# Kernel optimization log

Measured on AMD Instinct MI355X. Metric: run time of the kernel, lower is better.

## Reference

```python
import jax, jax.numpy as jnp
import numpy as np

NUM_HEADS = 16

def setup_inputs() -> dict:
    key = jax.random.key(0)
    ks = jax.random.split(key, 7)
    query_dim, kv_dim, out_dim = 1024, 768, 1024
    N, Lq, Lkv = 4, 2048, 2048
    s_q = 1.0 / np.sqrt(query_dim)
    s_kv = 1.0 / np.sqrt(kv_dim)
    return {
        "query": jax.random.normal(ks[0], (N, Lq, query_dim), dtype=jnp.float32),
        "kv": jax.random.normal(ks[1], (N, Lkv, kv_dim), dtype=jnp.float32),
        # Linear weights stored as (in_dim, out_dim) for x @ W
        "Wq": jax.random.uniform(ks[2], (query_dim, query_dim), jnp.float32, -s_q, s_q),
        "Wk": jax.random.uniform(ks[3], (kv_dim, query_dim), jnp.float32, -s_kv, s_kv),
        "Wv": jax.random.uniform(ks[4], (kv_dim, query_dim), jnp.float32, -s_kv, s_kv),
        "Wo": jax.random.uniform(ks[5], (query_dim, out_dim), jnp.float32, -s_q, s_q),
        "bo": jax.random.uniform(ks[6], (out_dim,), jnp.float32, -s_q, s_q),
    }

def reference(query, kv, Wq, Wk, Wv, Wo, bo):
    N, Lq, qd = query.shape
    Lkv = kv.shape[1]
    H = NUM_HEADS
    hd = qd // H
    scale = hd ** -0.5
    # projections -> (N, H, L, hd)
    q = (query @ Wq).reshape(N, Lq, H, hd).transpose(0, 2, 1, 3)
    k = (kv @ Wk).reshape(N, Lkv, H, hd).transpose(0, 2, 1, 3)
    v = (kv @ Wv).reshape(N, Lkv, H, hd).transpose(0, 2, 1, 3)
    # fp32 attention: (N, H, Lq, Lkv)
    attn = jnp.einsum('bhqd,bhkd->bhqk', q.astype(jnp.float32) * scale, k.astype(jnp.float32))
    attn = jax.nn.softmax(attn, axis=-1)
    out = jnp.einsum('bhqk,bhkd->bhqd', attn, v.astype(jnp.float32))
    out = out.transpose(0, 2, 1, 3).reshape(N, Lq, qd)
    return out @ Wo + bo
```

## Files before the change

### kernel.cpp

```cpp
#include <hip/hip_runtime.h>

typedef __attribute__((ext_vector_type(4))) float f32x4;
typedef __attribute__((ext_vector_type(8))) __bf16 bf16x8;
typedef __attribute__((ext_vector_type(8))) unsigned short us8;

__device__ __forceinline__ unsigned short f2bf(float f) {
    unsigned u = __builtin_bit_cast(unsigned, f);
    u += 0x7fffu + ((u >> 16) & 1u);
    return (unsigned short)(u >> 16);
}

__device__ __forceinline__ float exp2v(float x) {
    float r;
    asm("v_exp_f32 %0, %1" : "=v"(r) : "v"(x));
    return r;
}

__device__ __forceinline__ f32x4 mfma16(bf16x8 a, bf16x8 b, f32x4 c) {
    return __builtin_amdgcn_mfma_f32_16x16x32_bf16(a, b, c, 0, 0, 0);
}

__device__ __forceinline__ void gload16(const void* g, void* l) {
    __builtin_amdgcn_global_load_lds(
        (const __attribute__((address_space(1))) unsigned int*)g,
        (__attribute__((address_space(3))) unsigned int*)l, 16, 0, 0);
}

__global__ __launch_bounds__(256) void conv2_bf16(const float* __restrict__ a,
                                                  unsigned short* __restrict__ oa,
                                                  int na8,
                                                  const float* __restrict__ b,
                                                  unsigned short* __restrict__ ob,
                                                  int nb8) {
    int i = blockIdx.x * 256 + threadIdx.x;
    const float* in;
    unsigned short* out;
    if (i < na8) {
        in = a; out = oa;
    } else {
        i -= na8;
        if (i >= nb8) return;
        in = b; out = ob;
    }
    const float4* p = (const float4*)in + (size_t)i * 2;
    float4 x = p[0], y = p[1];
    us8 o;
    o[0] = f2bf(x.x); o[1] = f2bf(x.y); o[2] = f2bf(x.z); o[3] = f2bf(x.w);
    o[4] = f2bf(y.x); o[5] = f2bf(y.y); o[6] = f2bf(y.z); o[7] = f2bf(y.w);
    *((us8*)out + i) = o;
}

__global__ __launch_bounds__(256) void wtrans_all(const float* __restrict__ Wq,
                                                  const float* __restrict__ Wk,
                                                  const float* __restrict__ Wv,
                                                  const float* __restrict__ Wo,
                                                  unsigned short* __restrict__ WqT,
                                                  unsigned short* __restrict__ WkT,
                                                  unsigned short* __restrict__ WvT,
                                                  unsigned short* __restrict__ WoT,
                                                  float qscale) {
    __shared__ float t[32][33];
    int y = blockIdx.y;
    const float* in; unsigned short* out; int R; float scale = 1.0f;
    if (y < 32)      { in = Wq; out = WqT; R = 1024; scale = qscale; }
    else if (y < 56) { in = Wk; out = WkT; R = 768;  y -= 32; }
    else if (y < 80) { in = Wv; out = WvT; R = 768;  y -= 56; }
    else             { in = Wo; out = WoT; R = 1024; y -= 80; }
    int tx = threadIdx.x, ty = threadIdx.y;
    int r0 = y * 32, c0 = blockIdx.x * 32;
#pragma unroll
    for (int k = 0; k < 4; ++k)
        t[ty + k * 8][tx] = in[(size_t)(r0 + ty + k * 8) * 1024 + c0 + tx];
    __syncthreads();
#pragma unroll
    for (int k = 0; k < 4; ++k)
        out[(size_t)(c0 + ty + k * 8) * R + r0 + tx] = f2bf(t[tx][ty + k * 8] * scale);
}

template <int KD, int EPI>
__global__ __launch_bounds__(256, 4) void gemm_bf16(const unsigned short* __restrict__ A,
                                                    const unsigned short* __restrict__ B,
                                                    void* __restrict__ Cout,
                                                    const float* __restrict__ bias) {
    __shared__ __align__(16) unsigned short SL[2][8192];
    const int m0 = blockIdx.y * 128;
    const int n0 = blockIdx.x * 128;
    const int tid = threadIdx.x;
    const int w = tid >> 6, l = tid & 63;
    const int lr = l & 15, lg = l >> 4;
    const int wm = (w >> 1) * 64, wn = (w & 1) * 64;

    f32x4 acc[4][4] = {};

    int ci0 = w * 64 + l;
    int r0 = ci0 >> 2, c0 = (ci0 & 3) ^ (r0 & 3);
    int ci1 = 256 + ci0;
    int r1 = ci1 >> 2, c1 = (ci1 & 3) ^ (r1 & 3);

    const unsigned short* Ag0 = A + (size_t)(m0 + r0) * KD + c0 * 8;
    const unsigned short* Ag1 = A + (size_t)(m0 + r1) * KD + c1 * 8;
    const unsigned short* Bg0 = B + (size_t)(n0 + r0) * KD + c0 * 8;
    const unsigned short* Bg1 = B + (size_t)(n0 + r1) * KD + c1 * 8;

#define STG(buf, k0)                                                  \
    do {                                                              \
        gload16(Ag0 + (k0), &SL[buf][w * 512]);                       \
        gload16(Ag1 + (k0), &SL[buf][2048 + w * 512]);                \
        gload16(Bg0 + (k0), &SL[buf][4096 + w * 512]);                \
        gload16(Bg1 + (k0), &SL[buf][4096 + 2048 + w * 512]);         \
    } while (0)

    constexpr int NT = KD / 32;
    STG(0, 0);
    int buf = 0;
    for (int kt = 0; kt < NT; ++kt) {
        if (kt + 1 < NT) {
            STG(buf ^ 1, (kt + 1) * 32);
            asm volatile("s_waitcnt vmcnt(4)" ::: "memory");
        } else {
            asm volatile("s_waitcnt vmcnt(0)" ::: "memory");
        }
        __builtin_amdgcn_s_barrier();
        const unsigned short* Alc = &SL[buf][0];
        const unsigned short* Blc = &SL[buf][4096];
        bf16x8 af[4], bfr[4];
#pragma unroll
        for (int t = 0; t < 4; ++t) {
            int ar = wm + t * 16 + lr;
            af[t] = *(const bf16x8*)&Alc[ar * 32 + ((lg ^ (ar & 3)) * 8)];
            int br = wn + t * 16 + lr;
            bfr[t] = *(const bf16x8*)&Blc[br * 32 + ((lg ^ (br & 3)) * 8)];
        }
#pragma unroll
        for (int i = 0; i < 4; ++i)
#pragma unroll
            for (int j = 0; j < 4; ++j)
                acc[i][j] = mfma16(af[i], bfr[j], acc[i][j]);
        __builtin_amdgcn_s_barrier();
        buf ^= 1;
    }
#undef STG

#pragma unroll
    for (int i = 0; i < 4; ++i)
#pragma unroll
        for (int j = 0; j < 4; ++j)
#pragma unroll
            for (int r = 0; r < 4; ++r) {
                int m = m0 + wm + i * 16 + lg * 4 + r;
                int n = n0 + wn + j * 16 + lr;
                if (EPI == 0) {
                    int b = m >> 11, ql = m & 2047, h = n >> 6, d = n & 63;
                    ((unsigned short*)Cout)[(((size_t)(b * 16 + h) * 2048 + ql) << 6) + d] =
                        f2bf(acc[i][j][r]);
                } else {
                    ((float*)Cout)[(size_t)m * 1024 + n] = acc[i][j][r] + bias[n];
                }
            }
}

__global__ __launch_bounds__(256, 4) void gemm_kv(const unsigned short* __restrict__ A,
                                                  const unsigned short* __restrict__ Bk,
                                                  const unsigned short* __restrict__ Bv,
                                                  unsigned short* __restrict__ Ck,
                                                  unsigned short* __restrict__ Cv) {
    constexpr int KD = 768;
    __shared__ __align__(16) unsigned short SL[2][8192];
    const int isV = blockIdx.x >> 3;
    const int n0 = (blockIdx.x & 7) * 128;
    const int m0 = blockIdx.y * 128;
    const unsigned short* B = isV ? Bv : Bk;
    const int tid = threadIdx.x;
    const int w = tid >> 6, l = tid & 63;
    const int lr = l & 15, lg = l >> 4;
    const int wm = (w >> 1) * 64, wn = (w & 1) * 64;

    f32x4 acc[4][4] = {};

    int ci0 = w * 64 + l;
    int r0 = ci0 >> 2, c0 = (ci0 & 3) ^ (r0 & 3);
    int ci1 = 256 + ci0;
    int r1 = ci1 >> 2, c1 = (ci1 & 3) ^ (r1 & 3);

    const unsigned short* Ag0 = A + (size_t)(m0 + r0) * KD + c0 * 8;
    const unsigned short* Ag1 = A + (size_t)(m0 + r1) * KD + c1 * 8;
    const unsigned short* Bg0 = B + (size_t)(n0 + r0) * KD + c0 * 8;
    const unsigned short* Bg1 = B + (size_t)(n0 + r1) * KD + c1 * 8;

#define STG(buf, k0)                                                  \
    do {                                                              \
        gload16(Ag0 + (k0), &SL[buf][w * 512]);                       \
        gload16(Ag1 + (k0), &SL[buf][2048 + w * 512]);                \
        gload16(Bg0 + (k0), &SL[buf][4096 + w * 512]);                \
        gload16(Bg1 + (k0), &SL[buf][4096 + 2048 + w * 512]);         \
    } while (0)

    constexpr int NT = KD / 32;
    STG(0, 0);
    int buf = 0;
    for (int kt = 0; kt < NT; ++kt) {
        if (kt + 1 < NT) {
            STG(buf ^ 1, (kt + 1) * 32);
            asm volatile("s_waitcnt vmcnt(4)" ::: "memory");
        } else {
            asm volatile("s_waitcnt vmcnt(0)" ::: "memory");
        }
        __builtin_amdgcn_s_barrier();
        const unsigned short* Alc = &SL[buf][0];
        const unsigned short* Blc = &SL[buf][4096];
        bf16x8 af[4], bfr[4];
#pragma unroll
        for (int t = 0; t < 4; ++t) {
            int ar = wm + t * 16 + lr;
            af[t] = *(const bf16x8*)&Alc[ar * 32 + ((lg ^ (ar & 3)) * 8)];
            int br = wn + t * 16 + lr;
            bfr[t] = *(const bf16x8*)&Blc[br * 32 + ((lg ^ (br & 3)) * 8)];
        }
#pragma unroll
        for (int i = 0; i < 4; ++i)
#pragma unroll
            for (int j = 0; j < 4; ++j)
                acc[i][j] = mfma16(af[i], bfr[j], acc[i][j]);
        __builtin_amdgcn_s_barrier();
        buf ^= 1;
    }
#undef STG

    if (!isV) {
#pragma unroll
        for (int i = 0; i < 4; ++i)
#pragma unroll
            for (int j = 0; j < 4; ++j)
#pragma unroll
                for (int r = 0; r < 4; ++r) {
                    int m = m0 + wm + i * 16 + lg * 4 + r;
                    int n = n0 + wn + j * 16 + lr;
                    int b = m >> 11, ql = m & 2047, h = n >> 6, d = n & 63;
                    Ck[(((size_t)(b * 16 + h) * 2048 + ql) << 6) + d] = f2bf(acc[i][j][r]);
                }
    } else {
        const int b = m0 >> 11;
        const int mloc = m0 & 2047;
        const int h0 = n0 >> 6;
#pragma unroll
        for (int hp = 0; hp < 2; ++hp) {
            unsigned short* VTb = Cv + (size_t)(b * 16 + h0 + hp) * (64 * 2048);
#pragma unroll
            for (int dh = 0; dh < 2; ++dh) {
                __syncthreads();
                if ((w & 1) == hp) {
#pragma unroll
                    for (int jj = 0; jj < 2; ++jj) {
                        int j = dh * 2 + jj;
                        int dl = jj * 16 + lr;
#pragma unroll
                        for (int i = 0; i < 4; ++i)
#pragma unroll
                            for (int r = 0; r < 4; ++r) {
                                int kvl = wm + i * 16 + lg * 4 + r;
                                int pl = (kvl & 0x60) | (((kvl >> 2) & 3) << 3) |
                                         (((kvl >> 4) & 1) << 2) | (kvl & 3);
                                SL[0][dl * 136 + pl] = f2bf(acc[i][j][r]);
                            }
                    }
                }
                __syncthreads();
#pragma unroll
                for (int cc = 0; cc < 2; ++cc) {
                    int idx = cc * 256 + tid;
                    int row = idx >> 4, col = (idx & 15) * 8;
                    *(us8*)&VTb[(size_t)(dh * 32 + row) * 2048 + mloc + col] =
                        *(const us8*)&SL[0][row * 136 + col];
                }
            }
        }
    }
}

__global__ __launch_bounds__(256, 4) void attn_fwd(const unsigned short* __restrict__ Q,
                                                   const unsigned short* __restrict__ K,
                                                   const unsigned short* __restrict__ VT,
                                                   unsigned short* __restrict__ O) {
    __shared__ __align__(16) unsigned short Kl[2][64 * 64];
    __shared__ __align__(16) unsigned short Vl[2][64 * 64];
    const int id = blockIdx.x;
    const int sw = (id & 7) * 128 + (id >> 3);
    const int qt = sw & 15, bh = sw >> 4;
    const int tid = threadIdx.x;
    const int w = tid >> 6, l = tid & 63;
    const int lr = l & 15, lg = l >> 4;
    const size_t hbase = (size_t)bh * (2048 * 64);
    const size_t vbase = (size_t)bh * (64 * 2048);
    const int qbase = qt * 128 + w * 32;

    bf16x8 qf[2][2];
#pragma unroll
    for (int rt = 0; rt < 2; ++rt) {
        const unsigned short* qp = Q + hbase + (size_t)(qbase + rt * 16 + lr) * 64;
        qf[rt][0] = *(const bf16x8*)(qp + lg * 8);
        qf[rt][1] = *(const bf16x8*)(qp + 32 + lg * 8);
    }

    f32x4 oacc[2][4] = {};
    f32x4 lacc[2] = {};
    const f32x4 FZERO = {};

    bf16x8 ONES;
#pragma unroll
    for (int e = 0; e < 8; ++e) ONES[e] = (__bf16)1.0f;

    const int cA = tid, cB = 256 + tid;
    const int krA = cA >> 3, kcA = (cA & 7) ^ (krA & 7);
    const int krB = cB >> 3, kcB = (cB & 7) ^ (krB & 7);
    const unsigned short* Kg0 = K + hbase + (size_t)krA * 64 + kcA * 8;
    const unsigned short* Kg1 = K + hbase + (size_t)krB * 64 + kcB * 8;
    const unsigned short* Vg0 = VT + vbase + (size_t)krA * 2048 + kcA * 8;
    const unsigned short* Vg1 = VT + vbase + (size_t)krB * 2048 + kcB * 8;

#define STAGE_KV(dst, kv0)                                                    \
    do {                                                                      \
        gload16(Kg0 + (size_t)(kv0) * 64, &Kl[dst][w * 512]);                 \
        gload16(Kg1 + (size_t)(kv0) * 64, &Kl[dst][2048 + w * 512]);          \
        gload16(Vg0 + (kv0), &Vl[dst][w * 512]);                              \
        gload16(Vg1 + (kv0), &Vl[dst][2048 + w * 512]);                       \
    } while (0)

    const int koff0 = lr * 64 + ((lg ^ (lr & 7)) * 8);
    const int koff1 = lr * 64 + (((4 + lg) ^ (lr & 7)) * 8);

    STAGE_KV(0, 0);
    int cur = 0;

    for (int t = 0; t < 32; ++t) {
        if (t < 31) {
            STAGE_KV(cur ^ 1, (t + 1) * 64);
            asm volatile("s_waitcnt vmcnt(4)" ::: "memory");
        } else {
            asm volatile("s_waitcnt vmcnt(0)" ::: "memory");
        }
        __builtin_amdgcn_s_barrier();
        const unsigned short* Kc = Kl[cur];
        const unsigned short* Vc = Vl[cur];

        f32x4 s[2][4];
        __builtin_amdgcn_s_setprio(1);
#pragma unroll
        for (int nt = 0; nt < 4; ++nt) {
            bf16x8 kf0 = *(const bf16x8*)&Kc[koff0 + nt * 1024];
            bf16x8 kf1 = *(const bf16x8*)&Kc[koff1 + nt * 1024];
            s[0][nt] = mfma16(kf0, qf[0][0], FZERO);
            s[0][nt] = mfma16(kf1, qf[0][1], s[0][nt]);
            s[1][nt] = mfma16(kf0, qf[1][0], FZERO);
            s[1][nt] = mfma16(kf1, qf[1][1], s[1][nt]);
        }
        __builtin_amdgcn_s_setprio(0);

        bf16x8 pa0[2], pa1[2];
#pragma unroll
        for (int rt = 0; rt < 2; ++rt) {
#pragma unroll
            for (int nt = 0; nt < 4; ++nt)
#pragma unroll
                for (int r = 0; r < 4; ++r)
                    s[rt][nt][r] = exp2v(s[rt][nt][r]);
#pragma unroll
            for (int e = 0; e < 4; ++e) {
                pa0[rt][e] = (__bf16)s[rt][0][e];
                pa0[rt][4 + e] = (__bf16)s[rt][1][e];
                pa1[rt][e] = (__bf16)s[rt][2][e];
                pa1[rt][4 + e] = (__bf16)s[rt][3][e];
            }
        }

        __builtin_amdgcn_s_setprio(1);
        lacc[0] = mfma16(pa0[0], ONES, lacc[0]);
        lacc[0] = mfma16(pa1[0], ONES, lacc[0]);
        lacc[1] = mfma16(pa0[1], ONES, lacc[1]);
        lacc[1] = mfma16(pa1[1], ONES, lacc[1]);

#pragma unroll
        for (int nt = 0; nt < 4; ++nt) {
            bf16x8 vb0 = *(const bf16x8*)&Vc[koff0 + nt * 1024];
            bf16x8 vb1 = *(const bf16x8*)&Vc[koff1 + nt * 1024];
            oacc[0][nt] = mfma16(pa0[0], vb0, oacc[0][nt]);
            oacc[0][nt] = mfma16(pa1[0], vb1, oacc[0][nt]);
            oacc[1][nt] = mfma16(pa0[1], vb0, oacc[1][nt]);
            oacc[1][nt] = mfma16(pa1[1], vb1, oacc[1][nt]);
        }
        __builtin_amdgcn_s_setprio(0);
        __builtin_amdgcn_s_barrier();
        cur ^= 1;
    }
#undef STAGE_KV

    const int b = bh >> 4, h = bh & 15;
#pragma unroll
    for (int rt = 0; rt < 2; ++rt)
#pragma unroll
        for (int r = 0; r < 4; ++r) {
            float inv = 1.0f / lacc[rt][r];
            int q = qbase + rt * 16 + lg * 4 + r;
            size_t rowbase = ((size_t)(b * 2048 + q)) * 1024 + h * 64;
#pragma unroll
            for (int nt = 0; nt < 4; ++nt)
                O[rowbase + nt * 16 + lr] = f2bf(oacc[rt][nt][r] * inv);
        }
}

extern "C" void kernel_launch(void* const* d_in, const int* in_sizes, int n_in,
                              void* d_out, int out_size, void* d_ws, size_t ws_size,
                              hipStream_t stream) {
    (void)in_sizes; (void)n_in; (void)out_size; (void)ws_size;
    const float* query = (const float*)d_in[0];
    const float* kv    = (const float*)d_in[1];
    const float* Wq    = (const float*)d_in[2];
    const float* Wk    = (const float*)d_in[3];
    const float* Wv    = (const float*)d_in[4];
    const float* Wo    = (const float*)d_in[5];
    const float* bo    = (const float*)d_in[6];
    float* out = (float*)d_out;

    char* ws = (char*)d_ws;
    unsigned short* qbf  = (unsigned short*)(ws + 0);
    unsigned short* kvbf = (unsigned short*)(ws + 16777216);
    unsigned short* WkT  = (unsigned short*)(ws + 29360128);
    unsigned short* WvT  = (unsigned short*)(ws + 30932992);
    unsigned short* WqT  = (unsigned short*)(ws + 32505856);
    unsigned short* WoT  = (unsigned short*)(ws + 34603008);
    unsigned short* Qh   = (unsigned short*)(ws + 36700160);
    unsigned short* Kh   = (unsigned short*)(ws + 53477376);
    unsigned short* VTh  = (unsigned short*)(ws + 0);
    unsigned short* Ob   = (unsigned short*)(ws + 16777216);

    const float QSCALE = 0.18033688011112042f;

    conv2_bf16<<<7168, 256, 0, stream>>>(query, qbf, 1048576, kv, kvbf, 786432);
    wtrans_all<<<dim3(32, 112), dim3(32, 8), 0, stream>>>(Wq, Wk, Wv, Wo,
                                                          WqT, WkT, WvT, WoT, QSCALE);

    gemm_bf16<1024, 0><<<dim3(8, 64), 256, 0, stream>>>(qbf, WqT, Qh, nullptr);
    gemm_kv<<<dim3(16, 64), 256, 0, stream>>>(kvbf, WkT, WvT, Kh, VTh);
    attn_fwd<<<1024, 256, 0, stream>>>(Qh, Kh, VTh, Ob);
    gemm_bf16<1024, 1><<<dim3(8, 64), 256, 0, stream>>>(Ob, WoT, out, bo);
}
```

Measured before the change: 175.4 us.

## Merge Q/K/V projections into one 256x256-tile GEMM and fuse prep kernels

Replaces the separate Q GEMM and K/V GEMM with a single launch, proj8. It uses 512-thread blocks, 256x256 output tiles, BK=64 double-buffered LDS staging and XOR swizzling, and raises wave priority around the MFMA clusters. It also merges the bf16 conversion and weight-transpose kernels into one launch. The output GEMM gets an XCD-aware tile mapping. VT moves to its own workspace region because the projections now run concurrently. The larger tiles cut redundant global loads and launch overhead, but with one block per CU and 384 blocks the tail balance and occupancy may be worse.

```diff
diff --git a/kernel.cpp b/kernel.cpp
--- a/kernel.cpp
+++ b/kernel.cpp
@@ -26,65 +26,205 @@
         (__attribute__((address_space(3))) unsigned int*)l, 16, 0, 0);
 }
 
-__global__ __launch_bounds__(256) void conv2_bf16(const float* __restrict__ a,
-                                                  unsigned short* __restrict__ oa,
-                                                  int na8,
-                                                  const float* __restrict__ b,
-                                                  unsigned short* __restrict__ ob,
-                                                  int nb8) {
-    int i = blockIdx.x * 256 + threadIdx.x;
-    const float* in;
-    unsigned short* out;
-    if (i < na8) {
-        in = a; out = oa;
+__global__ __launch_bounds__(256) void prep(const float* __restrict__ query,
+                                            const float* __restrict__ kv,
+                                            const float* __restrict__ Wq,
+                                            const float* __restrict__ Wk,
+                                            const float* __restrict__ Wv,
+                                            const float* __restrict__ Wo,
+                                            unsigned short* __restrict__ qbf,
+                                            unsigned short* __restrict__ kvbf,
+                                            unsigned short* __restrict__ WqT,
+                                            unsigned short* __restrict__ WkT,
+                                            unsigned short* __restrict__ WvT,
+                                            unsigned short* __restrict__ WoT,
+                                            float qscale) {
+    __shared__ float t[32][33];
+    const int bid = blockIdx.x;
+    const int tid = threadIdx.x;
+    if (bid < 7168) {
+        int i = bid * 256 + tid;
+        const float* in;
+        unsigned short* out;
+        if (i < 1048576) {
+            in = query; out = qbf;
+        } else {
+            i -= 1048576;
+            if (i >= 786432) return;
+            in = kv; out = kvbf;
+        }
+        const float4* p = (const float4*)in + (size_t)i * 2;
+        float4 x = p[0], y = p[1];
+        us8 o;
+        o[0] = f2bf(x.x); o[1] = f2bf(x.y); o[2] = f2bf(x.z); o[3] = f2bf(x.w);
+        o[4] = f2bf(y.x); o[5] = f2bf(y.y); o[6] = f2bf(y.z); o[7] = f2bf(y.w);
+        *((us8*)out + i) = o;
     } else {
-        i -= na8;
-        if (i >= nb8) return;
-        in = b; out = ob;
-    }
-    const float4* p = (const float4*)in + (size_t)i * 2;
-    float4 x = p[0], y = p[1];
-    us8 o;
-    o[0] = f2bf(x.x); o[1] = f2bf(x.y); o[2] = f2bf(x.z); o[3] = f2bf(x.w);
-    o[4] = f2bf(y.x); o[5] = f2bf(y.y); o[6] = f2bf(y.z); o[7] = f2bf(y.w);
-    *((us8*)out + i) = o;
-}
-
-__global__ __launch_bounds__(256) void wtrans_all(const float* __restrict__ Wq,
-                                                  const float* __restrict__ Wk,
-                                                  const float* __restrict__ Wv,
-                                                  const float* __restrict__ Wo,
-                                                  unsigned short* __restrict__ WqT,
-                                                  unsigned short* __restrict__ WkT,
-                                                  unsigned short* __restrict__ WvT,
-                                                  unsigned short* __restrict__ WoT,
-                                                  float qscale) {
-    __shared__ float t[32][33];
-    int y = blockIdx.y;
-    const float* in; unsigned short* out; int R; float scale = 1.0f;
-    if (y < 32)      { in = Wq; out = WqT; R = 1024; scale = qscale; }
-    else if (y < 56) { in = Wk; out = WkT; R = 768;  y -= 32; }
-    else if (y < 80) { in = Wv; out = WvT; R = 768;  y -= 56; }
-    else             { in = Wo; out = WoT; R = 1024; y -= 80; }
-    int tx = threadIdx.x, ty = threadIdx.y;
-    int r0 = y * 32, c0 = blockIdx.x * 32;
-#pragma unroll
-    for (int k = 0; k < 4; ++k)
-        t[ty + k * 8][tx] = in[(size_t)(r0 + ty + k * 8) * 1024 + c0 + tx];
-    __syncthreads();
-#pragma unroll
-    for (int k = 0; k < 4; ++k)
-        out[(size_t)(c0 + ty + k * 8) * R + r0 + tx] = f2bf(t[tx][ty + k * 8] * scale);
-}
-
-template <int KD, int EPI>
-__global__ __launch_bounds__(256, 4) void gemm_bf16(const unsigned short* __restrict__ A,
-                                                    const unsigned short* __restrict__ B,
-                                                    void* __restrict__ Cout,
-                                                    const float* __restrict__ bias) {
+        int b2 = bid - 7168;
+        int c0 = (b2 & 31) * 32;
+        int y = b2 >> 5;
+        const float* in; unsigned short* out; int R; float scale = 1.0f;
+        if (y < 32)      { in = Wq; out = WqT; R = 1024; scale = qscale; }
+        else if (y < 56) { in = Wk; out = WkT; R = 768;  y -= 32; }
+        else if (y < 80) { in = Wv; out = WvT; R = 768;  y -= 56; }
+        else             { in = Wo; out = WoT; R = 1024; y -= 80; }
+        int tx = tid & 31, ty = tid >> 5;
+        int r0 = y * 32;
+#pragma unroll
+        for (int k = 0; k < 4; ++k)
+            t[ty + k * 8][tx] = in[(size_t)(r0 + ty + k * 8) * 1024 + c0 + tx];
+        __syncthreads();
+#pragma unroll
+        for (int k = 0; k < 4; ++k)
+            out[(size_t)(c0 + ty + k * 8) * R + r0 + tx] = f2bf(t[tx][ty + k * 8] * scale);
+    }
+}
+
+__global__ __launch_bounds__(512, 1) void proj8(const unsigned short* __restrict__ qbf,
+                                                const unsigned short* __restrict__ kvbf,
+                                                const unsigned short* __restrict__ WqT,
+                                                const unsigned short* __restrict__ WkT,
+                                                const unsigned short* __restrict__ WvT,
+                                                unsigned short* __restrict__ Qh,
+                                                unsigned short* __restrict__ Kh,
+                                                unsigned short* __restrict__ VTh) {
+    __shared__ __align__(16) unsigned short LDSall[65536];
+    const int id = blockIdx.x;
+    const int op = id >> 7;
+    const int t = id & 127;
+    const int xcd = t & 7, jj = t >> 3;
+    const int my = xcd * 4 + (jj & 3);
+    const int nx = jj >> 2;
+    const int m0 = my * 256, n0 = nx * 256;
+    const unsigned short* A = (op == 0) ? qbf : kvbf;
+    const unsigned short* B = (op == 0) ? WqT : (op == 1 ? WkT : WvT);
+    const int KD = (op == 0) ? 1024 : 768;
+    const int NT = KD >> 6;
+
+    const int tid = threadIdx.x;
+    const int w = tid >> 6, l = tid & 63;
+    const int lr = l & 15, lg = l >> 4;
+    const int wm = (w >> 2) * 128;
+    const int wn = (w & 3) * 64;
+
+    f32x4 acc[8][4] = {};
+
+    const int r0 = tid >> 3;
+    const int sc = (tid & 7) ^ (r0 & 7);
+    const unsigned short* Ag = A + (size_t)(m0 + r0) * KD + sc * 8;
+    const unsigned short* Bg = B + (size_t)(n0 + r0) * KD + sc * 8;
+
+#define STAGE8(buf, k0)                                                       \
+    do {                                                                      \
+        _Pragma("unroll")                                                     \
+        for (int p = 0; p < 4; ++p) {                                         \
+            gload16(Ag + (size_t)p * 64 * KD + (k0),                          \
+                    &LDSall[(buf) * 16384 + (p * 512 + tid) * 8]);            \
+            gload16(Bg + (size_t)p * 64 * KD + (k0),                          \
+                    &LDSall[32768 + (buf) * 16384 + (p * 512 + tid) * 8]);    \
+        }                                                                     \
+    } while (0)
+
+    const int c0 = ((lg ^ (lr & 7)) * 8);
+    const int c1 = (((4 + lg) ^ (lr & 7)) * 8);
+
+    STAGE8(0, 0);
+    int cur = 0;
+
+    for (int kt = 0; kt < NT; ++kt) {
+        asm volatile("s_waitcnt vmcnt(0)" ::: "memory");
+        __builtin_amdgcn_s_barrier();
+        if (kt + 1 < NT) STAGE8(cur ^ 1, (kt + 1) * 64);
+
+        const unsigned short* Ac = &LDSall[cur * 16384];
+        const unsigned short* Bc = &LDSall[32768 + cur * 16384];
+        bf16x8 bf[4][2];
+
+#pragma unroll
+        for (int p = 0; p < 4; ++p) {
+            bf16x8 a00, a01, a10, a11;
+            {
+                int ar0 = (wm + (2 * p) * 16 + lr) * 64;
+                int ar1 = (wm + (2 * p + 1) * 16 + lr) * 64;
+                a00 = *(const bf16x8*)&Ac[ar0 + c0];
+                a01 = *(const bf16x8*)&Ac[ar0 + c1];
+                a10 = *(const bf16x8*)&Ac[ar1 + c0];
+                a11 = *(const bf16x8*)&Ac[ar1 + c1];
+            }
+            if (p == 0) {
+#pragma unroll
+                for (int j = 0; j < 4; ++j) {
+                    int br = (wn + j * 16 + lr) * 64;
+                    bf[j][0] = *(const bf16x8*)&Bc[br + c0];
+                    bf[j][1] = *(const bf16x8*)&Bc[br + c1];
+                }
+            }
+            __builtin_amdgcn_s_barrier();
+            __builtin_amdgcn_s_setprio(1);
+#pragma unroll
+            for (int j = 0; j < 4; ++j) {
+                acc[2 * p][j] = mfma16(a00, bf[j][0], acc[2 * p][j]);
+                acc[2 * p][j] = mfma16(a01, bf[j][1], acc[2 * p][j]);
+                acc[2 * p + 1][j] = mfma16(a10, bf[j][0], acc[2 * p + 1][j]);
+                acc[2 * p + 1][j] = mfma16(a11, bf[j][1], acc[2 * p + 1][j]);
+            }
+            __builtin_amdgcn_s_setprio(0);
+            __builtin_amdgcn_s_barrier();
+        }
+        cur ^= 1;
+    }
+#undef STAGE8
+
+    if (op != 2) {
+        unsigned short* Cout = (op == 0) ? Qh : Kh;
+#pragma unroll
+        for (int i = 0; i < 8; ++i)
+#pragma unroll
+            for (int j = 0; j < 4; ++j)
+#pragma unroll
+                for (int r = 0; r < 4; ++r) {
+                    int m = m0 + wm + i * 16 + lg * 4 + r;
+                    int n = n0 + wn + j * 16 + lr;
+                    int b = m >> 11, ql = m & 2047, h = n >> 6, d = n & 63;
+                    Cout[(((size_t)(b * 16 + h) * 2048 + ql) << 6) + d] = f2bf(acc[i][j][r]);
+                }
+    } else {
+        unsigned short* scr = &LDSall[w * 8192];
+#pragma unroll
+        for (int i = 0; i < 8; ++i)
+#pragma unroll
+            for (int j = 0; j < 4; ++j)
+#pragma unroll
+                for (int r = 0; r < 4; ++r) {
+                    int kvl = i * 16 + lg * 4 + r;
+                    int pl = (kvl & 0x60) | (((kvl >> 2) & 3) << 3) |
+                             (((kvl >> 4) & 1) << 2) | (kvl & 3);
+                    scr[(j * 16 + lr) * 128 + pl] = f2bf(acc[i][j][r]);
+                }
+        const int b = m0 >> 11;
+        const int head = (n0 >> 6) + (w & 3);
+        const int mloc = (m0 & 2047) + wm;
+        unsigned short* VTb = VTh + (size_t)(b * 16 + head) * (64 * 2048);
+#pragma unroll
+        for (int kk = 0; kk < 16; ++kk) {
+            int drow = kk * 4 + (l >> 4);
+            int cchunk = (l & 15) * 8;
+            *(us8*)&VTb[(size_t)drow * 2048 + mloc + cchunk] =
+                *(const us8*)&scr[drow * 128 + cchunk];
+        }
+    }
+}
+
+__global__ __launch_bounds__(256, 4) void gemm_o(const unsigned short* __restrict__ A,
+                                                 const unsigned short* __restrict__ B,
+                                                 float* __restrict__ Cout,
+                                                 const float* __restrict__ bias) {
+    constexpr int KD = 1024;
     __shared__ __align__(16) unsigned short SL[2][8192];
-    const int m0 = blockIdx.y * 128;
-    const int n0 = blockIdx.x * 128;
+    const int id = blockIdx.x;
+    const int xcd = id & 7, j = id >> 3;
+    const int m0 = (xcd * 8 + (j & 7)) * 128;
+    const int n0 = (j >> 3) * 128;
     const int tid = threadIdx.x;
     const int w = tid >> 6, l = tid & 63;
     const int lr = l & 15, lg = l >> 4;
@@ -110,7 +250,7 @@
         gload16(Bg1 + (k0), &SL[buf][4096 + 2048 + w * 512]);         \
     } while (0)
 
-    constexpr int NT = KD / 32;
+    constexpr int NT = KD >> 5;
     STG(0, 0);
     int buf = 0;
     for (int kt = 0; kt < NT; ++kt) {
@@ -134,8 +274,8 @@
 #pragma unroll
         for (int i = 0; i < 4; ++i)
 #pragma unroll
-            for (int j = 0; j < 4; ++j)
-                acc[i][j] = mfma16(af[i], bfr[j], acc[i][j]);
+            for (int jj = 0; jj < 4; ++jj)
+                acc[i][jj] = mfma16(af[i], bfr[jj], acc[i][jj]);
         __builtin_amdgcn_s_barrier();
         buf ^= 1;
     }
@@ -144,137 +284,13 @@
 #pragma unroll
     for (int i = 0; i < 4; ++i)
 #pragma unroll
-        for (int j = 0; j < 4; ++j)
+        for (int jj = 0; jj < 4; ++jj)
 #pragma unroll
             for (int r = 0; r < 4; ++r) {
                 int m = m0 + wm + i * 16 + lg * 4 + r;
-                int n = n0 + wn + j * 16 + lr;
-                if (EPI == 0) {
-                    int b = m >> 11, ql = m & 2047, h = n >> 6, d = n & 63;
-                    ((unsigned short*)Cout)[(((size_t)(b * 16 + h) * 2048 + ql) << 6) + d] =
-                        f2bf(acc[i][j][r]);
-                } else {
-                    ((float*)Cout)[(size_t)m * 1024 + n] = acc[i][j][r] + bias[n];
-                }
+                int n = n0 + wn + jj * 16 + lr;
+                Cout[(size_t)m * 1024 + n] = acc[i][jj][r] + bias[n];
             }
-}
-
-__global__ __launch_bounds__(256, 4) void gemm_kv(const unsigned short* __restrict__ A,
-                                                  const unsigned short* __restrict__ Bk,
-                                                  const unsigned short* __restrict__ Bv,
-                                                  unsigned short* __restrict__ Ck,
-                                                  unsigned short* __restrict__ Cv) {
-    constexpr int KD = 768;
-    __shared__ __align__(16) unsigned short SL[2][8192];
-    const int isV = blockIdx.x >> 3;
-    const int n0 = (blockIdx.x & 7) * 128;
-    const int m0 = blockIdx.y * 128;
-    const unsigned short* B = isV ? Bv : Bk;
-    const int tid = threadIdx.x;
-    const int w = tid >> 6, l = tid & 63;
-    const int lr = l & 15, lg = l >> 4;
-    const int wm = (w >> 1) * 64, wn = (w & 1) * 64;
-
-    f32x4 acc[4][4] = {};
-
-    int ci0 = w * 64 + l;
-    int r0 = ci0 >> 2, c0 = (ci0 & 3) ^ (r0 & 3);
-    int ci1 = 256 + ci0;
-    int r1 = ci1 >> 2, c1 = (ci1 & 3) ^ (r1 & 3);
-
-    const unsigned short* Ag0 = A + (size_t)(m0 + r0) * KD + c0 * 8;
-    const unsigned short* Ag1 = A + (size_t)(m0 + r1) * KD + c1 * 8;
-    const unsigned short* Bg0 = B + (size_t)(n0 + r0) * KD + c0 * 8;
-    const unsigned short* Bg1 = B + (size_t)(n0 + r1) * KD + c1 * 8;
-
-#define STG(buf, k0)                                                  \
-    do {                                                              \
-        gload16(Ag0 + (k0), &SL[buf][w * 512]);                       \
-        gload16(Ag1 + (k0), &SL[buf][2048 + w * 512]);                \
-        gload16(Bg0 + (k0), &SL[buf][4096 + w * 512]);                \
-        gload16(Bg1 + (k0), &SL[buf][4096 + 2048 + w * 512]);         \
-    } while (0)
-
-    constexpr int NT = KD / 32;
-    STG(0, 0);
-    int buf = 0;
-    for (int kt = 0; kt < NT; ++kt) {
-        if (kt + 1 < NT) {
-            STG(buf ^ 1, (kt + 1) * 32);
-            asm volatile("s_waitcnt vmcnt(4)" ::: "memory");
-        } else {
-            asm volatile("s_waitcnt vmcnt(0)" ::: "memory");
-        }
-        __builtin_amdgcn_s_barrier();
-        const unsigned short* Alc = &SL[buf][0];
-        const unsigned short* Blc = &SL[buf][4096];
-        bf16x8 af[4], bfr[4];
-#pragma unroll
-        for (int t = 0; t < 4; ++t) {
-            int ar = wm + t * 16 + lr;
-            af[t] = *(const bf16x8*)&Alc[ar * 32 + ((lg ^ (ar & 3)) * 8)];
-            int br = wn + t * 16 + lr;
-            bfr[t] = *(const bf16x8*)&Blc[br * 32 + ((lg ^ (br & 3)) * 8)];
-        }
-#pragma unroll
-        for (int i = 0; i < 4; ++i)
-#pragma unroll
-            for (int j = 0; j < 4; ++j)
-                acc[i][j] = mfma16(af[i], bfr[j], acc[i][j]);
-        __builtin_amdgcn_s_barrier();
-        buf ^= 1;
-    }
-#undef STG
-
-    if (!isV) {
-#pragma unroll
-        for (int i = 0; i < 4; ++i)
-#pragma unroll
-            for (int j = 0; j < 4; ++j)
-#pragma unroll
-                for (int r = 0; r < 4; ++r) {
-                    int m = m0 + wm + i * 16 + lg * 4 + r;
-                    int n = n0 + wn + j * 16 + lr;
-                    int b = m >> 11, ql = m & 2047, h = n >> 6, d = n & 63;
-                    Ck[(((size_t)(b * 16 + h) * 2048 + ql) << 6) + d] = f2bf(acc[i][j][r]);
-                }
-    } else {
-        const int b = m0 >> 11;
-        const int mloc = m0 & 2047;
-        const int h0 = n0 >> 6;
-#pragma unroll
-        for (int hp = 0; hp < 2; ++hp) {
-            unsigned short* VTb = Cv + (size_t)(b * 16 + h0 + hp) * (64 * 2048);
-#pragma unroll
-            for (int dh = 0; dh < 2; ++dh) {
-                __syncthreads();
-                if ((w & 1) == hp) {
-#pragma unroll
-                    for (int jj = 0; jj < 2; ++jj) {
-                        int j = dh * 2 + jj;
-                        int dl = jj * 16 + lr;
-#pragma unroll
-                        for (int i = 0; i < 4; ++i)
-#pragma unroll
-                            for (int r = 0; r < 4; ++r) {
-                                int kvl = wm + i * 16 + lg * 4 + r;
-                                int pl = (kvl & 0x60) | (((kvl >> 2) & 3) << 3) |
-                                         (((kvl >> 4) & 1) << 2) | (kvl & 3);
-                                SL[0][dl * 136 + pl] = f2bf(acc[i][j][r]);
-                            }
-                    }
-                }
-                __syncthreads();
-#pragma unroll
-                for (int cc = 0; cc < 2; ++cc) {
-                    int idx = cc * 256 + tid;
-                    int row = idx >> 4, col = (idx & 15) * 8;
-                    *(us8*)&VTb[(size_t)(dh * 32 + row) * 2048 + mloc + col] =
-                        *(const us8*)&SL[0][row * 136 + col];
-                }
-            }
-        }
-    }
 }
 
 __global__ __launch_bounds__(256, 4) void attn_fwd(const unsigned short* __restrict__ Q,
@@ -429,17 +445,14 @@
     unsigned short* WoT  = (unsigned short*)(ws + 34603008);
     unsigned short* Qh   = (unsigned short*)(ws + 36700160);
     unsigned short* Kh   = (unsigned short*)(ws + 53477376);
-    unsigned short* VTh  = (unsigned short*)(ws + 0);
+    unsigned short* VTh  = (unsigned short*)(ws + 70254592);
     unsigned short* Ob   = (unsigned short*)(ws + 16777216);
 
     const float QSCALE = 0.18033688011112042f;
 
-    conv2_bf16<<<7168, 256, 0, stream>>>(query, qbf, 1048576, kv, kvbf, 786432);
-    wtrans_all<<<dim3(32, 112), dim3(32, 8), 0, stream>>>(Wq, Wk, Wv, Wo,
-                                                          WqT, WkT, WvT, WoT, QSCALE);
-
-    gemm_bf16<1024, 0><<<dim3(8, 64), 256, 0, stream>>>(qbf, WqT, Qh, nullptr);
-    gemm_kv<<<dim3(16, 64), 256, 0, stream>>>(kvbf, WkT, WvT, Kh, VTh);
+    prep<<<10752, 256, 0, stream>>>(query, kv, Wq, Wk, Wv, Wo,
+                                    qbf, kvbf, WqT, WkT, WvT, WoT, QSCALE);
+    proj8<<<384, 512, 0, stream>>>(qbf, kvbf, WqT, WkT, WvT, Qh, Kh, VTh);
     attn_fwd<<<1024, 256, 0, stream>>>(Qh, Kh, VTh, Ob);
-    gemm_bf16<1024, 1><<<dim3(8, 64), 256, 0, stream>>>(Ob, WoT, out, bo);
-}
+    gemm_o<<<512, 256, 0, stream>>>(Ob, WoT, out, bo);
+}
```

New measurement: 162.1 us. 7.6% less time.
